# Kernel tuning notes

Hardware: AMD Instinct MI355X
Metric: run time of the kernel (lower is better)

Reference implementation:

```python
import jax, jax.numpy as jnp
import numpy as np

B, L, C = 2048, 200, 100
DID, DTXT, DCTX, K, V = 64, 128, 128, 5, 2000
DIN = DID + DTXT
HID = 128


def setup_inputs() -> dict:
    ks = jax.random.split(jax.random.key(0), 20)
    g = lambda i, s: jax.random.normal(ks[i], s, jnp.float32) * 0.05
    z = lambda *s: jnp.zeros(s, jnp.float32)
    return {
        "seq_items": jax.random.randint(ks[0], (B, L), 0, V),
        "seq_id_emb": jax.random.normal(ks[1], (B, L, DID), jnp.float32),
        "seq_text_emb": jax.random.normal(ks[2], (B, L, DTXT), jnp.float32),
        "lengths": K + jax.random.randint(ks[3], (B,), 0, L - K + 1),  # ensure >= K
        "cand_ids": jax.random.randint(ks[4], (B, C), 0, V),
        "cand_id_emb": jax.random.normal(ks[5], (B, C, DID), jnp.float32),
        "cand_text_emb": jax.random.normal(ks[6], (B, C, DTXT), jnp.float32),
        "co_table": jax.random.uniform(ks[7], (V, V), jnp.float32),  # dense cooccur_dict
        "W_ih": g(8, (3 * DCTX, DIN)), "W_hh": g(9, (3 * DCTX, DCTX)),
        "b_ih": z(3 * DCTX), "b_hh": z(3 * DCTX),
        "Wt1": g(10, (HID, 2 * DTXT + DCTX)), "bt1": z(HID),
        "Wt2": g(11, (1, HID)), "bt2": z(1),
        "Wi1": g(12, (HID, 2 * DID + DCTX)), "bi1": z(HID),
        "Wi2": g(13, (1, HID)), "bi2": z(1),
        "Wa1": g(14, (64, DCTX)), "ba1": z(64),
        "Wa2": g(15, (3, 64)), "ba2": z(3),
        "Wstab": g(16, (1, DIN)),
        "beta_c": jnp.float32(1.0),
        "logT_c": jnp.float32(0.0), "logT_t": jnp.float32(0.0), "logT_id": jnp.float32(0.0),
    }


def _gru_last(xk, W_ih, W_hh, b_ih, b_hh):
    """Torch-convention single-layer GRU over [B,K,Din]; returns last hidden [B,H]."""
    def step(h, x_t):
        i_r, i_z, i_n = jnp.split(x_t @ W_ih.T + b_ih, 3, axis=-1)
        h_r, h_z, h_n = jnp.split(h @ W_hh.T + b_hh, 3, axis=-1)
        r = jax.nn.sigmoid(i_r + h_r)
        zg = jax.nn.sigmoid(i_z + h_z)
        n = jnp.tanh(i_n + r * h_n)
        return (1.0 - zg) * n + zg * h, None
    h0 = jnp.zeros((xk.shape[0], W_hh.shape[1]), xk.dtype)
    h, _ = jax.lax.scan(step, h0, jnp.swapaxes(xk, 0, 1))
    return h


def _scorer(e_src, e_tgt, h, W1, b1, W2, b2):
    Bc, Cc = e_tgt.shape[:2]
    x = jnp.concatenate([
        jnp.broadcast_to(e_src[:, None, :], (Bc, Cc, e_src.shape[-1])),
        e_tgt,
        jnp.broadcast_to(h[:, None, :], (Bc, Cc, h.shape[-1])),
    ], axis=-1)  # [B,C,2*Dsrc+DCTX]
    return (jax.nn.relu(x @ W1.T + b1) @ W2.T + b2)[..., 0]  # [B,C]


def _forward(seq_items, seq_id_emb, seq_text_emb, lengths, cand_ids, cand_id_emb,
             cand_text_emb, co_table, W_ih, W_hh, b_ih, b_hh, Wt1, bt1, Wt2, bt2,
             Wi1, bi1, Wi2, bi2, Wa1, ba1, Wa2, ba2, Wstab, beta_c,
             logT_c, logT_t, logT_id):
    seq_in = jnp.concatenate([seq_id_emb, seq_text_emb], axis=-1)  # [B,L,DIN]
    b_idx = jnp.arange(seq_in.shape[0])
    # vectorized last-k window gather (lengths >= K by construction)
    win = (lengths - K)[:, None] + jnp.arange(K)[None, :]          # [B,K]
    xk = jnp.take_along_axis(seq_in, win[:, :, None], axis=1)      # [B,K,DIN]
    h = _gru_last(xk, W_ih, W_hh, b_ih, b_hh)                      # [B,DCTX]
    last = lengths - 1
    last_id = seq_id_emb[b_idx, last]                              # [B,DID]
    last_text = seq_text_emb[b_idx, last]                          # [B,DTXT]
    # co-occurrence view: dense-table lookup replacing the Python dict loop
    last_item = seq_items[b_idx, last]                             # [B]
    co_scores = co_table[last_item[:, None], cand_ids]             # [B,C]
    P_c = jax.nn.softmax(beta_c * co_scores / jnp.exp(logT_c), axis=-1)
    P_t = jax.nn.softmax(_scorer(last_text, cand_text_emb, h, Wt1, bt1, Wt2, bt2) / jnp.exp(logT_t), axis=-1)
    P_id = jax.nn.softmax(_scorer(last_id, cand_id_emb, h, Wi1, bi1, Wi2, bi2) / jnp.exp(logT_id), axis=-1)
    alpha = jax.nn.softmax(jax.nn.relu(h @ Wa1.T + ba1) @ Wa2.T + ba2, axis=-1)  # [B,3]
    P_mix_ns = alpha[:, 0:1] * P_c + alpha[:, 1:2] * P_t + alpha[:, 2:3] * P_id
    stable = seq_in.mean(axis=1) @ Wstab.T                         # [B,1]
    P_stable = jax.nn.softmax(jnp.broadcast_to(stable, P_mix_ns.shape), axis=-1)
    P_mix = jnp.clip(P_stable + P_mix_ns, 1e-12, None)
    return P_mix / P_mix.sum(axis=-1, keepdims=True)


def reference(seq_items, seq_id_emb, seq_text_emb, lengths, cand_ids, cand_id_emb,
              cand_text_emb, co_table, W_ih, W_hh, b_ih, b_hh, Wt1, bt1, Wt2, bt2,
              Wi1, bi1, Wi2, bi2, Wa1, ba1, Wa2, ba2, Wstab, beta_c,
              logT_c, logT_t, logT_id):
    return _forward(seq_items, seq_id_emb, seq_text_emb, lengths, cand_ids,
                    cand_id_emb, cand_text_emb, co_table, W_ih, W_hh, b_ih, b_hh,
                    Wt1, bt1, Wt2, bt2, Wi1, bi1, Wi2, bi2, Wa1, ba1, Wa2, ba2,
                    Wstab, beta_c, logT_c, logT_t, logT_id)
```

## Files before the change

### kernel.cpp

```cpp
#include <hip/hip_runtime.h>
#include <hip/hip_bf16.h>

constexpr int B_   = 2048;
constexpr int L_   = 200;
constexpr int C_   = 100;
constexpr int DID_ = 64;
constexpr int DTXT_= 128;
constexpr int DCTX_= 128;
constexpr int KWIN = 5;
constexpr int V_   = 2000;
constexpr int DIN_ = DID_ + DTXT_;
constexpr int HID_ = 128;
constexpr int TB   = 4;


__global__ __launch_bounds__(256) void k0_transpose(
    const float* __restrict__ W_ih, const float* __restrict__ W_hh,
    const float* __restrict__ Wt1,  const float* __restrict__ Wi1,
    const float* __restrict__ Wa1,
    float* __restrict__ WihT,  float* __restrict__ WhhT,
    float* __restrict__ Wt1uT, float* __restrict__ Wt1sT,
    float* __restrict__ Wi1uT, float* __restrict__ Wi1sT,
    float* __restrict__ Wa1T)
{
  int idx = blockIdx.x*256 + threadIdx.x;
  int stride = gridDim.x*256;
  for (int i = idx; i < 192*384; i += stride) {
    int k = i/384, r = i%384; WihT[i] = W_ih[r*192 + k];
  }
  for (int i = idx; i < 128*384; i += stride) {
    int k = i/384, r = i%384; WhhT[i] = W_hh[r*128 + k];
  }
  for (int i = idx; i < 256*128; i += stride) {
    int k = i/128, j = i%128;
    Wt1uT[i] = (k < 128) ? Wt1[j*384 + k] : Wt1[j*384 + 256 + (k-128)];
  }
  for (int i = idx; i < 128*128; i += stride) {
    int k = i/128, j = i%128; Wt1sT[i] = Wt1[j*384 + 128 + k];
  }
  for (int i = idx; i < 192*128; i += stride) {
    int k = i/128, j = i%128;
    Wi1uT[i] = (k < 64) ? Wi1[j*256 + k] : Wi1[j*256 + 128 + (k-64)];
  }
  for (int i = idx; i < 64*128; i += stride) {
    int k = i/128, j = i%128; Wi1sT[i] = Wi1[j*256 + 64 + k];
  }
  for (int i = idx; i < 128*64; i += stride) {
    int k = i/64, u = i%64; Wa1T[i] = Wa1[u*128 + k];
  }
}

__device__ __forceinline__ float sigm(float x) { return 1.f/(1.f + __expf(-x)); }

__global__ __launch_bounds__(256) void k1_gru(
    const int*   __restrict__ lengths,
    const float* __restrict__ seq_id,
    const float* __restrict__ seq_text,
    const float* __restrict__ WihT, const float* __restrict__ WhhT,
    const float* __restrict__ b_ih, const float* __restrict__ b_hh,
    const float* __restrict__ Wt1uT, const float* __restrict__ bt1,
    const float* __restrict__ Wi1uT, const float* __restrict__ bi1,
    const float* __restrict__ Wa1T,  const float* __restrict__ ba1,
    const float* __restrict__ Wa2,   const float* __restrict__ ba2,
    float* __restrict__ u_t, float* __restrict__ u_i,
    float* __restrict__ alp)
{
  __shared__ float xk[TB][KWIN][DIN_];
  __shared__ float G[KWIN*TB*384];
  __shared__ float Hacc[TB][384];
  __shared__ float hbuf[2][TB][DCTX_];
  __shared__ float ltext[TB][DTXT_];
  __shared__ float lid[TB][DID_];
  __shared__ float a1s[TB][64];
  __shared__ int   s_start[TB], s_last[TB];

  const int tid = threadIdx.x;
  const int b0  = blockIdx.x * TB;

  if (tid < TB) {
    int len = lengths[b0 + tid];
    s_start[tid] = len - KWIN;
    s_last[tid]  = len - 1;
  }
  __syncthreads();

  for (int i = tid; i < TB*KWIN*(DID_/4); i += 256) {
    int bb = i/(KWIN*16), r = i%(KWIN*16), t = r/16, q = r%16;
    ((float4*)&xk[bb][t][0])[q] =
      ((const float4*)(seq_id + ((size_t)(b0+bb)*L_ + s_start[bb]+t)*DID_))[q];
  }
  for (int i = tid; i < TB*KWIN*(DTXT_/4); i += 256) {
    int bb = i/(KWIN*32), r = i%(KWIN*32), t = r/32, q = r%32;
    ((float4*)&xk[bb][t][DID_])[q] =
      ((const float4*)(seq_text + ((size_t)(b0+bb)*L_ + s_start[bb]+t)*DTXT_))[q];
  }
  for (int i = tid; i < TB*(DTXT_/4); i += 256) {
    int bb = i/32, q = i%32;
    ((float4*)ltext[bb])[q] =
      ((const float4*)(seq_text + ((size_t)(b0+bb)*L_ + s_last[bb])*DTXT_))[q];
  }
  for (int i = tid; i < TB*(DID_/4); i += 256) {
    int bb = i/16, q = i%16;
    ((float4*)lid[bb])[q] =
      ((const float4*)(seq_id + ((size_t)(b0+bb)*L_ + s_last[bb])*DID_))[q];
  }
  for (int i = tid; i < TB*DCTX_; i += 256) ((float*)hbuf[0])[i] = 0.f;
  __syncthreads();

  if (tid < 192) {
    const int r0 = 2*tid;
    float acc[KWIN][TB][2];
    const float bi0 = b_ih[r0], bi1v = b_ih[r0+1];
    #pragma unroll
    for (int t = 0; t < KWIN; ++t)
      #pragma unroll
      for (int bb = 0; bb < TB; ++bb) { acc[t][bb][0] = bi0; acc[t][bb][1] = bi1v; }
    const float* w = WihT + r0;
    for (int k4 = 0; k4 < DIN_; k4 += 4) {
      float2 w0 = *(const float2*)&w[(size_t)(k4+0)*384];
      float2 w1 = *(const float2*)&w[(size_t)(k4+1)*384];
      float2 w2 = *(const float2*)&w[(size_t)(k4+2)*384];
      float2 w3 = *(const float2*)&w[(size_t)(k4+3)*384];
      #pragma unroll
      for (int t = 0; t < KWIN; ++t)
        #pragma unroll
        for (int bb = 0; bb < TB; ++bb) {
          float4 x = *(const float4*)&xk[bb][t][k4];
          acc[t][bb][0] += w0.x*x.x + w1.x*x.y + w2.x*x.z + w3.x*x.w;
          acc[t][bb][1] += w0.y*x.x + w1.y*x.y + w2.y*x.z + w3.y*x.w;
        }
    }
    #pragma unroll
    for (int t = 0; t < KWIN; ++t)
      #pragma unroll
      for (int bb = 0; bb < TB; ++bb) {
        float2 o; o.x = acc[t][bb][0]; o.y = acc[t][bb][1];
        *(float2*)&G[(size_t)(t*TB+bb)*384 + r0] = o;
      }
  }
  __syncthreads();

  int cur = 0;
  for (int t = 0; t < KWIN; ++t) {
    if (tid < 192) {
      const int r0 = 2*tid;
      float acc[TB][2];
      const float bh0 = b_hh[r0], bh1 = b_hh[r0+1];
      #pragma unroll
      for (int bb = 0; bb < TB; ++bb) { acc[bb][0] = bh0; acc[bb][1] = bh1; }
      const float* w = WhhT + r0;
      for (int k4 = 0; k4 < DCTX_; k4 += 4) {
        float2 w0 = *(const float2*)&w[(size_t)(k4+0)*384];
        float2 w1 = *(const float2*)&w[(size_t)(k4+1)*384];
        float2 w2 = *(const float2*)&w[(size_t)(k4+2)*384];
        float2 w3 = *(const float2*)&w[(size_t)(k4+3)*384];
        #pragma unroll
        for (int bb = 0; bb < TB; ++bb) {
          float4 x = *(const float4*)&hbuf[cur][bb][k4];
          acc[bb][0] += w0.x*x.x + w1.x*x.y + w2.x*x.z + w3.x*x.w;
          acc[bb][1] += w0.y*x.x + w1.y*x.y + w2.y*x.z + w3.y*x.w;
        }
      }
      #pragma unroll
      for (int bb = 0; bb < TB; ++bb) {
        float2 o; o.x = acc[bb][0]; o.y = acc[bb][1];
        *(float2*)&Hacc[bb][r0] = o;
      }
    }
    __syncthreads();
    {
      const int j   = tid & 127;
      const int bb0 = (tid >> 7) * 2;
      #pragma unroll
      for (int e = 0; e < 2; ++e) {
        int bb = bb0 + e;
        const float* g = &G[(size_t)(t*TB+bb)*384];
        float i_r = g[j], i_z = g[128+j], i_n = g[256+j];
        float h_r = Hacc[bb][j], h_z = Hacc[bb][128+j], h_n = Hacc[bb][256+j];
        float r  = sigm(i_r + h_r);
        float zg = sigm(i_z + h_z);
        float n  = tanhf(i_n + r*h_n);
        hbuf[1-cur][bb][j] = (1.f - zg)*n + zg*hbuf[cur][bb][j];
      }
    }
    __syncthreads();
    cur ^= 1;
  }
  const float (*hf)[DCTX_] = hbuf[cur];

  if (tid < 64) {
    const int j0 = 2*tid;
    float acc[TB][2];
    const float bb0v = bt1[j0], bb1v = bt1[j0+1];
    #pragma unroll
    for (int bb = 0; bb < TB; ++bb) { acc[bb][0] = bb0v; acc[bb][1] = bb1v; }
    const float* w = Wt1uT + j0;
    for (int k4 = 0; k4 < 128; k4 += 4) {
      float2 w0 = *(const float2*)&w[(size_t)(k4+0)*128];
      float2 w1 = *(const float2*)&w[(size_t)(k4+1)*128];
      float2 w2 = *(const float2*)&w[(size_t)(k4+2)*128];
      float2 w3 = *(const float2*)&w[(size_t)(k4+3)*128];
      #pragma unroll
      for (int bb = 0; bb < TB; ++bb) {
        float4 x = *(const float4*)&ltext[bb][k4];
        acc[bb][0] += w0.x*x.x + w1.x*x.y + w2.x*x.z + w3.x*x.w;
        acc[bb][1] += w0.y*x.x + w1.y*x.y + w2.y*x.z + w3.y*x.w;
      }
    }
    for (int k4 = 0; k4 < 128; k4 += 4) {
      float2 w0 = *(const float2*)&w[(size_t)(128+k4+0)*128];
      float2 w1 = *(const float2*)&w[(size_t)(128+k4+1)*128];
      float2 w2 = *(const float2*)&w[(size_t)(128+k4+2)*128];
      float2 w3 = *(const float2*)&w[(size_t)(128+k4+3)*128];
      #pragma unroll
      for (int bb = 0; bb < TB; ++bb) {
        float4 x = *(const float4*)&hf[bb][k4];
        acc[bb][0] += w0.x*x.x + w1.x*x.y + w2.x*x.z + w3.x*x.w;
        acc[bb][1] += w0.y*x.x + w1.y*x.y + w2.y*x.z + w3.y*x.w;
      }
    }
    #pragma unroll
    for (int bb = 0; bb < TB; ++bb) {
      float2 o; o.x = acc[bb][0]; o.y = acc[bb][1];
      *(float2*)&u_t[((size_t)b0+bb)*HID_ + j0] = o;
    }
  } else if (tid < 128) {
    const int j0 = 2*(tid-64);
    float acc[TB][2];
    const float bb0v = bi1[j0], bb1v = bi1[j0+1];
    #pragma unroll
    for (int bb = 0; bb < TB; ++bb) { acc[bb][0] = bb0v; acc[bb][1] = bb1v; }
    const float* w = Wi1uT + j0;
    for (int k4 = 0; k4 < 64; k4 += 4) {
      float2 w0 = *(const float2*)&w[(size_t)(k4+0)*128];
      float2 w1 = *(const float2*)&w[(size_t)(k4+1)*128];
      float2 w2 = *(const float2*)&w[(size_t)(k4+2)*128];
      float2 w3 = *(const float2*)&w[(size_t)(k4+3)*128];
      #pragma unroll
      for (int bb = 0; bb < TB; ++bb) {
        float4 x = *(const float4*)&lid[bb][k4];
        acc[bb][0] += w0.x*x.x + w1.x*x.y + w2.x*x.z + w3.x*x.w;
        acc[bb][1] += w0.y*x.x + w1.y*x.y + w2.y*x.z + w3.y*x.w;
      }
    }
    for (int k4 = 0; k4 < 128; k4 += 4) {
      float2 w0 = *(const float2*)&w[(size_t)(64+k4+0)*128];
      float2 w1 = *(const float2*)&w[(size_t)(64+k4+1)*128];
      float2 w2 = *(const float2*)&w[(size_t)(64+k4+2)*128];
      float2 w3 = *(const float2*)&w[(size_t)(64+k4+3)*128];
      #pragma unroll
      for (int bb = 0; bb < TB; ++bb) {
        float4 x = *(const float4*)&hf[bb][k4];
        acc[bb][0] += w0.x*x.x + w1.x*x.y + w2.x*x.z + w3.x*x.w;
        acc[bb][1] += w0.y*x.x + w1.y*x.y + w2.y*x.z + w3.y*x.w;
      }
    }
    #pragma unroll
    for (int bb = 0; bb < TB; ++bb) {
      float2 o; o.x = acc[bb][0]; o.y = acc[bb][1];
      *(float2*)&u_i[((size_t)b0+bb)*HID_ + j0] = o;
    }
  } else if (tid < 160) {
    const int u0 = 2*(tid-128);
    float acc[TB][2];
    const float bb0v = ba1[u0], bb1v = ba1[u0+1];
    #pragma unroll
    for (int bb = 0; bb < TB; ++bb) { acc[bb][0] = bb0v; acc[bb][1] = bb1v; }
    const float* w = Wa1T + u0;
    for (int k4 = 0; k4 < 128; k4 += 4) {
      float2 w0 = *(const float2*)&w[(size_t)(k4+0)*64];
      float2 w1 = *(const float2*)&w[(size_t)(k4+1)*64];
      float2 w2 = *(const float2*)&w[(size_t)(k4+2)*64];
      float2 w3 = *(const float2*)&w[(size_t)(k4+3)*64];
      #pragma unroll
      for (int bb = 0; bb < TB; ++bb) {
        float4 x = *(const float4*)&hf[bb][k4];
        acc[bb][0] += w0.x*x.x + w1.x*x.y + w2.x*x.z + w3.x*x.w;
        acc[bb][1] += w0.y*x.x + w1.y*x.y + w2.y*x.z + w3.y*x.w;
      }
    }
    #pragma unroll
    for (int bb = 0; bb < TB; ++bb) {
      a1s[bb][u0]   = fmaxf(acc[bb][0], 0.f);
      a1s[bb][u0+1] = fmaxf(acc[bb][1], 0.f);
    }
  }
  __syncthreads();
  if (tid < TB) {
    int bb = tid;
    float lg0 = ba2[0], lg1 = ba2[1], lg2 = ba2[2];
    for (int k = 0; k < 64; ++k) {
      float a = a1s[bb][k];
      lg0 += Wa2[k]*a; lg1 += Wa2[64+k]*a; lg2 += Wa2[128+k]*a;
    }
    float m  = fmaxf(lg0, fmaxf(lg1, lg2));
    float e0 = __expf(lg0-m), e1 = __expf(lg1-m), e2 = __expf(lg2-m);
    float inv = 1.f/(e0+e1+e2);
    alp[((size_t)b0+bb)*3+0] = e0*inv;
    alp[((size_t)b0+bb)*3+1] = e1*inv;
    alp[((size_t)b0+bb)*3+2] = e2*inv;
  }
}

__global__ __launch_bounds__(256) void k2_score(
    const int*   __restrict__ seq_items,
    const int*   __restrict__ lengths,
    const int*   __restrict__ cand_ids,
    const float* __restrict__ cand_id_emb,
    const float* __restrict__ cand_text_emb,
    const float* __restrict__ co_table,
    const float* __restrict__ Wt1sT, const float* __restrict__ Wt2,
    const float* __restrict__ Wi1sT, const float* __restrict__ Wi2,
    const float* __restrict__ u_t, const float* __restrict__ u_i,
    const float* __restrict__ alp,
    const float* __restrict__ beta_c, const float* __restrict__ logT_c,
    const float* __restrict__ logT_t, const float* __restrict__ logT_id,
    float* __restrict__ out)
{
  __shared__ float Et[C_][DTXT_];
  __shared__ float Ei[C_][DID_];
  __shared__ float ut_s[HID_], ui_s[HID_], wt2_s[HID_], wi2_s[HID_];
  __shared__ float sc[3][C_];
  __shared__ float invsum_s;

  const int tid = threadIdx.x;
  const int b   = blockIdx.x;

  {
    const float4* src = (const float4*)(cand_text_emb + (size_t)b*C_*DTXT_);
    float4* dst = (float4*)Et;
    for (int i = tid; i < C_*DTXT_/4; i += 256) dst[i] = src[i];
    const float4* src2 = (const float4*)(cand_id_emb + (size_t)b*C_*DID_);
    float4* dst2 = (float4*)Ei;
    for (int i = tid; i < C_*DID_/4; i += 256) dst2[i] = src2[i];
  }
  if (tid < HID_) {
    ut_s[tid]  = u_t[(size_t)b*HID_ + tid];
    ui_s[tid]  = u_i[(size_t)b*HID_ + tid];
    wt2_s[tid] = Wt2[tid];
    wi2_s[tid] = Wi2[tid];
  }
  {
    int last_item = seq_items[(size_t)b*L_ + (lengths[b]-1)];
    float scale_c = beta_c[0] * __expf(-logT_c[0]);
    for (int c = tid; c < C_; c += 256) {
      int cid = cand_ids[(size_t)b*C_ + c];
      sc[0][c] = co_table[(size_t)last_item*V_ + cid] * scale_c;
    }
  }
  __syncthreads();

  const int jq = tid & 31, cg = tid >> 5, j0 = jq*4;
  const float invTt = __expf(-logT_t[0]);
  const float invTi = __expf(-logT_id[0]);

  for (int p = 0; p < 4; ++p) {
    int cbase = p*32 + cg*4;
    float acc[4][4];
    #pragma unroll
    for (int cc = 0; cc < 4; ++cc)
      #pragma unroll
      for (int jj = 0; jj < 4; ++jj) acc[cc][jj] = 0.f;
    const float* x0 = Et[(cbase+0) < C_ ? cbase+0 : C_-1];
    const float* x1 = Et[(cbase+1) < C_ ? cbase+1 : C_-1];
    const float* x2 = Et[(cbase+2) < C_ ? cbase+2 : C_-1];
    const float* x3 = Et[(cbase+3) < C_ ? cbase+3 : C_-1];
    const float* w  = Wt1sT + j0;
    for (int k4 = 0; k4 < 128; k4 += 4) {
      float4 w0 = *(const float4*)&w[(size_t)(k4+0)*128];
      float4 w1 = *(const float4*)&w[(size_t)(k4+1)*128];
      float4 w2 = *(const float4*)&w[(size_t)(k4+2)*128];
      float4 w3 = *(const float4*)&w[(size_t)(k4+3)*128];
      float4 xa = *(const float4*)&x0[k4];
      float4 xb = *(const float4*)&x1[k4];
      float4 xc = *(const float4*)&x2[k4];
      float4 xd = *(const float4*)&x3[k4];
      #pragma unroll
      for (int jj = 0; jj < 4; ++jj) {
        float wva = (&w0.x)[jj], wvb = (&w1.x)[jj], wvc = (&w2.x)[jj], wvd = (&w3.x)[jj];
        acc[0][jj] += wva*xa.x + wvb*xa.y + wvc*xa.z + wvd*xa.w;
        acc[1][jj] += wva*xb.x + wvb*xb.y + wvc*xb.z + wvd*xb.w;
        acc[2][jj] += wva*xc.x + wvb*xc.y + wvc*xc.z + wvd*xc.w;
        acc[3][jj] += wva*xd.x + wvb*xd.y + wvc*xd.z + wvd*xd.w;
      }
    }
    #pragma unroll
    for (int cc = 0; cc < 4; ++cc) {
      float s = wt2_s[j0+0]*fmaxf(acc[cc][0]+ut_s[j0+0], 0.f)
              + wt2_s[j0+1]*fmaxf(acc[cc][1]+ut_s[j0+1], 0.f)
              + wt2_s[j0+2]*fmaxf(acc[cc][2]+ut_s[j0+2], 0.f)
              + wt2_s[j0+3]*fmaxf(acc[cc][3]+ut_s[j0+3], 0.f);
      s += __shfl_xor(s,16); s += __shfl_xor(s,8); s += __shfl_xor(s,4);
      s += __shfl_xor(s,2);  s += __shfl_xor(s,1);
      int c = cbase + cc;
      if (jq == 0 && c < C_) sc[1][c] = s * invTt;
    }
  }

  for (int p = 0; p < 4; ++p) {
    int cbase = p*32 + cg*4;
    float acc[4][4];
    #pragma unroll
    for (int cc = 0; cc < 4; ++cc)
      #pragma unroll
      for (int jj = 0; jj < 4; ++jj) acc[cc][jj] = 0.f;
    const float* x0 = Ei[(cbase+0) < C_ ? cbase+0 : C_-1];
    const float* x1 = Ei[(cbase+1) < C_ ? cbase+1 : C_-1];
    const float* x2 = Ei[(cbase+2) < C_ ? cbase+2 : C_-1];
    const float* x3 = Ei[(cbase+3) < C_ ? cbase+3 : C_-1];
    const float* w  = Wi1sT + j0;
    for (int k4 = 0; k4 < 64; k4 += 4) {
      float4 w0 = *(const float4*)&w[(size_t)(k4+0)*128];
      float4 w1 = *(const float4*)&w[(size_t)(k4+1)*128];
      float4 w2 = *(const float4*)&w[(size_t)(k4+2)*128];
      float4 w3 = *(const float4*)&w[(size_t)(k4+3)*128];
      float4 xa = *(const float4*)&x0[k4];
      float4 xb = *(const float4*)&x1[k4];
      float4 xc = *(const float4*)&x2[k4];
      float4 xd = *(const float4*)&x3[k4];
      #pragma unroll
      for (int jj = 0; jj < 4; ++jj) {
        float wva = (&w0.x)[jj], wvb = (&w1.x)[jj], wvc = (&w2.x)[jj], wvd = (&w3.x)[jj];
        acc[0][jj] += wva*xa.x + wvb*xa.y + wvc*xa.z + wvd*xa.w;
        acc[1][jj] += wva*xb.x + wvb*xb.y + wvc*xb.z + wvd*xb.w;
        acc[2][jj] += wva*xc.x + wvb*xc.y + wvc*xc.z + wvd*xc.w;
        acc[3][jj] += wva*xd.x + wvb*xd.y + wvc*xd.z + wvd*xd.w;
      }
    }
    #pragma unroll
    for (int cc = 0; cc < 4; ++cc) {
      float s = wi2_s[j0+0]*fmaxf(acc[cc][0]+ui_s[j0+0], 0.f)
              + wi2_s[j0+1]*fmaxf(acc[cc][1]+ui_s[j0+1], 0.f)
              + wi2_s[j0+2]*fmaxf(acc[cc][2]+ui_s[j0+2], 0.f)
              + wi2_s[j0+3]*fmaxf(acc[cc][3]+ui_s[j0+3], 0.f);
      s += __shfl_xor(s,16); s += __shfl_xor(s,8); s += __shfl_xor(s,4);
      s += __shfl_xor(s,2);  s += __shfl_xor(s,1);
      int c = cbase + cc;
      if (jq == 0 && c < C_) sc[2][c] = s * invTi;
    }
  }
  __syncthreads();

  const int wv = tid >> 6, lane = tid & 63;
  if (wv < 3) {
    float* s = sc[wv];
    float v0 = s[lane];
    float v1 = (lane+64 < C_) ? s[lane+64] : -3.0e38f;
    float m = fmaxf(v0, v1);
    #pragma unroll
    for (int msk = 32; msk >= 1; msk >>= 1) m = fmaxf(m, __shfl_xor(m, msk));
    float e0 = __expf(v0 - m);
    float e1 = (lane+64 < C_) ? __expf(v1 - m) : 0.f;
    float su = e0 + e1;
    #pragma unroll
    for (int msk = 32; msk >= 1; msk >>= 1) su += __shfl_xor(su, msk);
    float inv = 1.f/su;
    s[lane] = e0*inv;
    if (lane+64 < C_) s[lane+64] = e1*inv;
  }
  __syncthreads();

  const float a0 = alp[(size_t)b*3+0];
  const float a1 = alp[(size_t)b*3+1];
  const float a2 = alp[(size_t)b*3+2];
  float v = 0.f;
  float* vals = &Et[0][0];
  if (tid < C_) {
    v = 0.01f + a0*sc[0][tid] + a1*sc[1][tid] + a2*sc[2][tid];
    vals[tid] = v;
  }
  __syncthreads();
  if (tid < 64) {
    float x = vals[tid] + ((tid+64 < C_) ? vals[tid+64] : 0.f);
    #pragma unroll
    for (int msk = 32; msk >= 1; msk >>= 1) x += __shfl_xor(x, msk);
    if (tid == 0) invsum_s = 1.f/x;
  }
  __syncthreads();
  if (tid < C_) out[(size_t)b*C_ + tid] = v * invsum_s;
}

extern "C" void kernel_launch(void* const* d_in, const int* in_sizes, int n_in,
                              void* d_out, int out_size, void* d_ws, size_t ws_size,
                              hipStream_t stream) {
  const int*   seq_items     = (const int*)  d_in[0];
  const float* seq_id_emb    = (const float*)d_in[1];
  const float* seq_text_emb  = (const float*)d_in[2];
  const int*   lengths       = (const int*)  d_in[3];
  const int*   cand_ids      = (const int*)  d_in[4];
  const float* cand_id_emb   = (const float*)d_in[5];
  const float* cand_text_emb = (const float*)d_in[6];
  const float* co_table      = (const float*)d_in[7];
  const float* W_ih          = (const float*)d_in[8];
  const float* W_hh          = (const float*)d_in[9];
  const float* b_ih          = (const float*)d_in[10];
  const float* b_hh          = (const float*)d_in[11];
  const float* Wt1           = (const float*)d_in[12];
  const float* bt1           = (const float*)d_in[13];
  const float* Wt2           = (const float*)d_in[14];
  const float* Wi1           = (const float*)d_in[16];
  const float* bi1           = (const float*)d_in[17];
  const float* Wi2           = (const float*)d_in[18];
  const float* Wa1           = (const float*)d_in[20];
  const float* ba1           = (const float*)d_in[21];
  const float* Wa2           = (const float*)d_in[22];
  const float* ba2           = (const float*)d_in[23];
  const float* beta_c        = (const float*)d_in[25];
  const float* logT_c        = (const float*)d_in[26];
  const float* logT_t        = (const float*)d_in[27];
  const float* logT_id       = (const float*)d_in[28];
  float* out = (float*)d_out;

  float* p = (float*)d_ws;
  float* u_t   = p; p += (size_t)B_*HID_;
  float* u_i   = p; p += (size_t)B_*HID_;
  float* alp   = p; p += (size_t)B_*3;
  float* WihT  = p; p += 192*384;
  float* WhhT  = p; p += 128*384;
  float* Wt1uT = p; p += 256*128;
  float* Wt1sT = p; p += 128*128;
  float* Wi1uT = p; p += 192*128;
  float* Wi1sT = p; p += 64*128;
  float* Wa1T  = p; p += 128*64;

  k0_transpose<<<128, 256, 0, stream>>>(
      W_ih, W_hh, Wt1, Wi1, Wa1,
      WihT, WhhT, Wt1uT, Wt1sT, Wi1uT, Wi1sT, Wa1T);

  k1_gru<<<B_/TB, 256, 0, stream>>>(
      lengths, seq_id_emb, seq_text_emb,
      WihT, WhhT, b_ih, b_hh,
      Wt1uT, bt1, Wi1uT, bi1, Wa1T, ba1, Wa2, ba2,
      u_t, u_i, alp);

  k2_score<<<B_, 256, 0, stream>>>(
      seq_items, lengths, cand_ids,
      cand_id_emb, cand_text_emb, co_table,
      Wt1sT, Wt2, Wi1sT, Wi2,
      u_t, u_i, alp,
      beta_c, logT_c, logT_t, logT_id,
      out);
}
```

Before: 733.5 us.

## Read candidate embeddings directly from global memory in scoring kernel, drop LDS staging

```diff
diff --git a/kernel.cpp b/kernel.cpp
--- a/kernel.cpp
+++ b/kernel.cpp
@@ -302,6 +302,39 @@
   }
 }
 
+template<int CC, int KD>
+__device__ __forceinline__ void score_chunk(
+    const float* __restrict__ xb,
+    const float* __restrict__ wT,
+    int j0, int lane,
+    float u0, float u1, float w20, float w21,
+    float invT, float* __restrict__ out)
+{
+  float acc0[CC], acc1[CC];
+  #pragma unroll
+  for (int c = 0; c < CC; ++c) { acc0[c] = 0.f; acc1[c] = 0.f; }
+  for (int k4 = 0; k4 < KD; k4 += 4) {
+    float2 w0 = *(const float2*)&wT[(size_t)(k4+0)*128 + j0];
+    float2 w1 = *(const float2*)&wT[(size_t)(k4+1)*128 + j0];
+    float2 w2 = *(const float2*)&wT[(size_t)(k4+2)*128 + j0];
+    float2 w3 = *(const float2*)&wT[(size_t)(k4+3)*128 + j0];
+    #pragma unroll
+    for (int c = 0; c < CC; ++c) {
+      float4 x = *(const float4*)&xb[(size_t)c*KD + k4];
+      acc0[c] += w0.x*x.x + w1.x*x.y + w2.x*x.z + w3.x*x.w;
+      acc1[c] += w0.y*x.x + w1.y*x.y + w2.y*x.z + w3.y*x.w;
+    }
+  }
+  #pragma unroll
+  for (int c = 0; c < CC; ++c) {
+    float s = w20*fmaxf(acc0[c] + u0, 0.f)
+            + w21*fmaxf(acc1[c] + u1, 0.f);
+    s += __shfl_xor(s, 32); s += __shfl_xor(s, 16); s += __shfl_xor(s, 8);
+    s += __shfl_xor(s, 4);  s += __shfl_xor(s, 2);  s += __shfl_xor(s, 1);
+    if (lane == 0) out[c] = s * invT;
+  }
+}
+
 __global__ __launch_bounds__(256) void k2_score(
     const int*   __restrict__ seq_items,
     const int*   __restrict__ lengths,
@@ -317,29 +350,16 @@
     const float* __restrict__ logT_t, const float* __restrict__ logT_id,
     float* __restrict__ out)
 {
-  __shared__ float Et[C_][DTXT_];
-  __shared__ float Ei[C_][DID_];
-  __shared__ float ut_s[HID_], ui_s[HID_], wt2_s[HID_], wi2_s[HID_];
-  __shared__ float sc[3][C_];
+  __shared__ float sc[3][128];
+  __shared__ float vals[128];
   __shared__ float invsum_s;
 
-  const int tid = threadIdx.x;
-  const int b   = blockIdx.x;
-
-  {
-    const float4* src = (const float4*)(cand_text_emb + (size_t)b*C_*DTXT_);
-    float4* dst = (float4*)Et;
-    for (int i = tid; i < C_*DTXT_/4; i += 256) dst[i] = src[i];
-    const float4* src2 = (const float4*)(cand_id_emb + (size_t)b*C_*DID_);
-    float4* dst2 = (float4*)Ei;
-    for (int i = tid; i < C_*DID_/4; i += 256) dst2[i] = src2[i];
-  }
-  if (tid < HID_) {
-    ut_s[tid]  = u_t[(size_t)b*HID_ + tid];
-    ui_s[tid]  = u_i[(size_t)b*HID_ + tid];
-    wt2_s[tid] = Wt2[tid];
-    wi2_s[tid] = Wi2[tid];
-  }
+  const int tid  = threadIdx.x;
+  const int b    = blockIdx.x;
+  const int lane = tid & 63;
+  const int wv   = tid >> 6;
+  const int j0   = lane * 2;
+
   {
     int last_item = seq_items[(size_t)b*L_ + (lengths[b]-1)];
     float scale_c = beta_c[0] * __expf(-logT_c[0]);
@@ -348,100 +368,24 @@
       sc[0][c] = co_table[(size_t)last_item*V_ + cid] * scale_c;
     }
   }
-  __syncthreads();
-
-  const int jq = tid & 31, cg = tid >> 5, j0 = jq*4;
+
   const float invTt = __expf(-logT_t[0]);
   const float invTi = __expf(-logT_id[0]);
-
-  for (int p = 0; p < 4; ++p) {
-    int cbase = p*32 + cg*4;
-    float acc[4][4];
-    #pragma unroll
-    for (int cc = 0; cc < 4; ++cc)
-      #pragma unroll
-      for (int jj = 0; jj < 4; ++jj) acc[cc][jj] = 0.f;
-    const float* x0 = Et[(cbase+0) < C_ ? cbase+0 : C_-1];
-    const float* x1 = Et[(cbase+1) < C_ ? cbase+1 : C_-1];
-    const float* x2 = Et[(cbase+2) < C_ ? cbase+2 : C_-1];
-    const float* x3 = Et[(cbase+3) < C_ ? cbase+3 : C_-1];
-    const float* w  = Wt1sT + j0;
-    for (int k4 = 0; k4 < 128; k4 += 4) {
-      float4 w0 = *(const float4*)&w[(size_t)(k4+0)*128];
-      float4 w1 = *(const float4*)&w[(size_t)(k4+1)*128];
-      float4 w2 = *(const float4*)&w[(size_t)(k4+2)*128];
-      float4 w3 = *(const float4*)&w[(size_t)(k4+3)*128];
-      float4 xa = *(const float4*)&x0[k4];
-      float4 xb = *(const float4*)&x1[k4];
-      float4 xc = *(const float4*)&x2[k4];
-      float4 xd = *(const float4*)&x3[k4];
-      #pragma unroll
-      for (int jj = 0; jj < 4; ++jj) {
-        float wva = (&w0.x)[jj], wvb = (&w1.x)[jj], wvc = (&w2.x)[jj], wvd = (&w3.x)[jj];
-        acc[0][jj] += wva*xa.x + wvb*xa.y + wvc*xa.z + wvd*xa.w;
-        acc[1][jj] += wva*xb.x + wvb*xb.y + wvc*xb.z + wvd*xb.w;
-        acc[2][jj] += wva*xc.x + wvb*xc.y + wvc*xc.z + wvd*xc.w;
-        acc[3][jj] += wva*xd.x + wvb*xd.y + wvc*xd.z + wvd*xd.w;
-      }
-    }
-    #pragma unroll
-    for (int cc = 0; cc < 4; ++cc) {
-      float s = wt2_s[j0+0]*fmaxf(acc[cc][0]+ut_s[j0+0], 0.f)
-              + wt2_s[j0+1]*fmaxf(acc[cc][1]+ut_s[j0+1], 0.f)
-              + wt2_s[j0+2]*fmaxf(acc[cc][2]+ut_s[j0+2], 0.f)
-              + wt2_s[j0+3]*fmaxf(acc[cc][3]+ut_s[j0+3], 0.f);
-      s += __shfl_xor(s,16); s += __shfl_xor(s,8); s += __shfl_xor(s,4);
-      s += __shfl_xor(s,2);  s += __shfl_xor(s,1);
-      int c = cbase + cc;
-      if (jq == 0 && c < C_) sc[1][c] = s * invTt;
-    }
-  }
-
-  for (int p = 0; p < 4; ++p) {
-    int cbase = p*32 + cg*4;
-    float acc[4][4];
-    #pragma unroll
-    for (int cc = 0; cc < 4; ++cc)
-      #pragma unroll
-      for (int jj = 0; jj < 4; ++jj) acc[cc][jj] = 0.f;
-    const float* x0 = Ei[(cbase+0) < C_ ? cbase+0 : C_-1];
-    const float* x1 = Ei[(cbase+1) < C_ ? cbase+1 : C_-1];
-    const float* x2 = Ei[(cbase+2) < C_ ? cbase+2 : C_-1];
-    const float* x3 = Ei[(cbase+3) < C_ ? cbase+3 : C_-1];
-    const float* w  = Wi1sT + j0;
-    for (int k4 = 0; k4 < 64; k4 += 4) {
-      float4 w0 = *(const float4*)&w[(size_t)(k4+0)*128];
-      float4 w1 = *(const float4*)&w[(size_t)(k4+1)*128];
-      float4 w2 = *(const float4*)&w[(size_t)(k4+2)*128];
-      float4 w3 = *(const float4*)&w[(size_t)(k4+3)*128];
-      float4 xa = *(const float4*)&x0[k4];
-      float4 xb = *(const float4*)&x1[k4];
-      float4 xc = *(const float4*)&x2[k4];
-      float4 xd = *(const float4*)&x3[k4];
-      #pragma unroll
-      for (int jj = 0; jj < 4; ++jj) {
-        float wva = (&w0.x)[jj], wvb = (&w1.x)[jj], wvc = (&w2.x)[jj], wvd = (&w3.x)[jj];
-        acc[0][jj] += wva*xa.x + wvb*xa.y + wvc*xa.z + wvd*xa.w;
-        acc[1][jj] += wva*xb.x + wvb*xb.y + wvc*xb.z + wvd*xb.w;
-        acc[2][jj] += wva*xc.x + wvb*xc.y + wvc*xc.z + wvd*xc.w;
-        acc[3][jj] += wva*xd.x + wvb*xd.y + wvc*xd.z + wvd*xd.w;
-      }
-    }
-    #pragma unroll
-    for (int cc = 0; cc < 4; ++cc) {
-      float s = wi2_s[j0+0]*fmaxf(acc[cc][0]+ui_s[j0+0], 0.f)
-              + wi2_s[j0+1]*fmaxf(acc[cc][1]+ui_s[j0+1], 0.f)
-              + wi2_s[j0+2]*fmaxf(acc[cc][2]+ui_s[j0+2], 0.f)
-              + wi2_s[j0+3]*fmaxf(acc[cc][3]+ui_s[j0+3], 0.f);
-      s += __shfl_xor(s,16); s += __shfl_xor(s,8); s += __shfl_xor(s,4);
-      s += __shfl_xor(s,2);  s += __shfl_xor(s,1);
-      int c = cbase + cc;
-      if (jq == 0 && c < C_) sc[2][c] = s * invTi;
-    }
-  }
-  __syncthreads();
-
-  const int wv = tid >> 6, lane = tid & 63;
+  const float ut0 = u_t[(size_t)b*HID_ + j0], ut1 = u_t[(size_t)b*HID_ + j0 + 1];
+  const float ui0 = u_i[(size_t)b*HID_ + j0], ui1 = u_i[(size_t)b*HID_ + j0 + 1];
+  const float wt20 = Wt2[j0], wt21 = Wt2[j0+1];
+  const float wi20 = Wi2[j0], wi21 = Wi2[j0+1];
+
+  const int c0 = wv * 25;
+  const float* Et_base = cand_text_emb + ((size_t)b*C_ + c0)*DTXT_;
+  const float* Ei_base = cand_id_emb   + ((size_t)b*C_ + c0)*DID_;
+
+  score_chunk<13, DTXT_>(Et_base,            Wt1sT, j0, lane, ut0, ut1, wt20, wt21, invTt, &sc[1][c0]);
+  score_chunk<12, DTXT_>(Et_base + 13*DTXT_, Wt1sT, j0, lane, ut0, ut1, wt20, wt21, invTt, &sc[1][c0+13]);
+  score_chunk<13, DID_ >(Ei_base,            Wi1sT, j0, lane, ui0, ui1, wi20, wi21, invTi, &sc[2][c0]);
+  score_chunk<12, DID_ >(Ei_base + 13*DID_,  Wi1sT, j0, lane, ui0, ui1, wi20, wi21, invTi, &sc[2][c0+13]);
+  __syncthreads();
+
   if (wv < 3) {
     float* s = sc[wv];
     float v0 = s[lane];
@@ -464,7 +408,6 @@
   const float a1 = alp[(size_t)b*3+1];
   const float a2 = alp[(size_t)b*3+2];
   float v = 0.f;
-  float* vals = &Et[0][0];
   if (tid < C_) {
     v = 0.01f + a0*sc[0][tid] + a1*sc[1][tid] + a2*sc[2][tid];
     vals[tid] = v;
```

Measured after the change: 973.8 us. +32.8%, slower.
